# Kernel tuning notes

Hardware: AMD Instinct MI355X
Metric: run time of the kernel (lower is better)

## Reference

```python
import jax, jax.numpy as jnp
import numpy as np

N = 50_000          # nodes
E = 1_600_000       # edges (avg degree 32)
S_IN, V_IN = 128, 16
S_OUT, V_OUT = 128, 16
HID = max(V_IN, V_OUT)   # bottleneck=1 -> hidden = max(v_in, v_out)
SVO = 3                  # scalarization_vectorization_output_dim
EPS = 1e-8               # safe_norm eps


def setup_inputs() -> dict:
    key = jax.random.key(0)
    ks = jax.random.split(key, 12)
    scale = 0.05
    return {
        "scalar": jax.random.normal(ks[0], (N, S_IN), jnp.float32),
        "vector": jax.random.normal(ks[1], (N, V_IN, 3), jnp.float32),
        "edge_index": jax.random.randint(ks[2], (2, E), 0, N, jnp.int32),
        "frames": jax.random.normal(ks[3], (E, 3, 3), jnp.float32),
        # parameters (torch Linear convention: W has shape (out, in))
        "W_down": jax.random.normal(ks[4], (HID, V_IN), jnp.float32) * scale,
        "W_df": jax.random.normal(ks[5], (SVO, V_IN), jnp.float32) * scale,
        "W_so": jax.random.normal(ks[6], (S_OUT, HID + S_IN + 3 * SVO), jnp.float32) * scale,
        "b_so": jax.random.normal(ks[7], (S_OUT,), jnp.float32) * scale,
        "W_up": jax.random.normal(ks[8], (V_OUT, HID), jnp.float32) * scale,
        "W_g": jax.random.normal(ks[9], (V_OUT, S_OUT), jnp.float32) * scale,
        "b_g": jax.random.normal(ks[10], (V_OUT,), jnp.float32) * scale,
    }


def _scalarize(vdf, edge_index, frames, dim_size):
    # vdf: (N, 3xyz, SVO) node-wise down-projected vectors.
    # Gather source-node vectors per edge, rotate into each edge's local frame,
    # then scatter-mean back to source nodes (node_inputs=True path).
    row = edge_index[0]
    vi = vdf[row]                                    # (E, 3, SVO)
    local = jnp.einsum('eij,ejc->eic', frames, vi)   # project onto frame rows
    local = jnp.swapaxes(local, -1, -2).reshape(vi.shape[0], 3 * SVO)  # (E, 9)
    sums = jax.ops.segment_sum(local, row, num_segments=dim_size)
    cnt = jax.ops.segment_sum(jnp.ones((vi.shape[0],), local.dtype), row,
                              num_segments=dim_size)
    return sums / jnp.maximum(cnt, 1.0)[:, None]     # scatter mean, 0 for empty


def reference(scalar, vector, edge_index, frames,
              W_down, W_df, W_so, b_so, W_up, W_g, b_g):
    silu = jax.nn.silu
    v_pre = jnp.swapaxes(vector, -1, -2)             # (N, 3, V_IN)
    vh = v_pre @ W_down.T                            # (N, 3, HID) vector_down
    vnorm = jnp.sqrt(jnp.sum(vh * vh, axis=-2) + EPS)  # safe_norm over xyz -> (N, HID)
    vdf = v_pre @ W_df.T                             # (N, 3, SVO) vector_down_frames
    sh = _scalarize(vdf, edge_index, frames, scalar.shape[0])  # (N, 9)
    merged = jnp.concatenate([scalar, vnorm, sh], axis=-1)     # (N, S_IN+HID+9)
    s = merged @ W_so.T + b_so                       # (N, S_OUT) scalar_out
    # vector branch (vector_gate=True, frame_gate=False, no residual)
    vrep = jnp.swapaxes(vh @ W_up.T, -1, -2)         # (N, V_OUT, 3)
    gate = silu(s) @ W_g.T + b_g                     # (N, V_OUT)
    vrep = vrep * jax.nn.sigmoid(gate)[..., None]
    return silu(s), vrep
```

## Files before the change

kernel.cpp:

```cpp
#include <hip/hip_runtime.h>

typedef unsigned short ushort_t;
typedef __attribute__((ext_vector_type(4))) unsigned short bfx4;
typedef __attribute__((ext_vector_type(8))) unsigned short bfx8;
typedef __attribute__((ext_vector_type(8))) short sfx8;
typedef __attribute__((ext_vector_type(4))) float fx4;

#define NABLK  512
#define RTH    1024
#define KBMAX  52
#define CAPL   60
#define FLC    16
#define RD     6
#define QMAX   224
#define SPN    8
#define ATB    512

#define FXS 4194304.0f
#define FXONE (1 << 22)

__device__ __forceinline__ float bf2f(unsigned short u){
  unsigned int x = ((unsigned int)u) << 16;
  float f; __builtin_memcpy(&f, &x, 4); return f;
}
__device__ __forceinline__ unsigned short f2bf(float f){
  unsigned int x; __builtin_memcpy(&x, &f, 4);
  x += 0x7fffu + ((x >> 16) & 1u);
  return (unsigned short)(x >> 16);
}
__device__ __forceinline__ int f2fx(float v){ return __float2int_rn(v * FXS); }
__device__ __forceinline__ unsigned short f2h(float f){
  _Float16 h = (_Float16)f;
  unsigned short u; __builtin_memcpy(&u, &h, 2); return u;
}
__device__ __forceinline__ float h2f(unsigned int u16){
  unsigned short us = (unsigned short)u16;
  _Float16 h; __builtin_memcpy(&h, &us, 2); return (float)h;
}
__device__ __forceinline__ unsigned int pk2(float a, float b){
  return (unsigned int)f2h(a) | ((unsigned int)f2h(b) << 16);
}

__global__ __launch_bounds__(256) void k_prep(const float* __restrict__ wso,
                                              ushort_t* __restrict__ wpk,
                                              float* __restrict__ sums, int N10)
{
  int gid = blockIdx.x * 256 + threadIdx.x;
  int b4 = gid * 4;
  if (b4 + 4 <= N10){
    fx4 z = {0.f, 0.f, 0.f, 0.f};
    *(fx4*)(sums + b4) = z;
  } else if (b4 < N10){
    for (int t = b4; t < N10; t++) sums[t] = 0.f;
  }
  if (gid < 8*5*64*8){
    int j    = gid & 7;
    int lane = (gid >> 3) & 63;
    int ks   = (gid >> 9) % 5;
    int nt   = gid / 2560;
    int mrow = lane & 15, quad = lane >> 4;
    int o = nt*16 + mrow;
    int k = ks*32 + quad*8 + j;
    float v = (k < 153) ? wso[o*153 + k] : 0.f;
    wpk[gid] = f2bf(v);
  }
}

__global__ void k_edge(const int* __restrict__ ei, const float* __restrict__ frames,
                       float* __restrict__ sums, int E)
{
  int e = blockIdx.x * 256 + threadIdx.x;
  if (e >= E) return;
  int row = ei[e];
  const float* fp = frames + (size_t)e * 9;
  float F[9];
  __builtin_memcpy(F, fp, 36);
  float* sp = sums + (size_t)row * 10;
  #pragma unroll
  for (int t = 0; t < 9; t++) atomicAdd(&sp[t], F[t]);
  atomicAdd(&sp[9], 1.0f);
}

__global__ __launch_bounds__(RTH) void k_part(const int* __restrict__ ei,
                                              const float* __restrict__ frames,
                                              unsigned int* __restrict__ recs,
                                              int* __restrict__ counts,
                                              float* __restrict__ sums,
                                              int E, int EPB, int KB, int CAPG)
{
  __shared__ unsigned int s_buf[KBMAX * CAPL * RD];
  __shared__ int s_cnt[KBMAX];
  __shared__ int s_gof[KBMAX];
  __shared__ int s_cap[KBMAX];
  __shared__ int s_qb[QMAX];
  __shared__ int s_qd[QMAX];
  __shared__ int s_nq;

  const int tid  = threadIdx.x;
  const int ablk = blockIdx.x;
  const int e0 = ablk * EPB;
  const int e1 = min(e0 + EPB, E);

  for (int b = tid; b < KB; b += RTH){ s_cnt[b] = 0; s_gof[b] = 0; s_cap[b] = CAPG; }
  if (tid == 0) s_nq = 0;
  __syncthreads();

  for (int i0 = e0; i0 < e1; i0 += RTH){
    int e = i0 + tid;
    if (e < e1){
      int row = ei[e];
      float F[9];
      __builtin_memcpy(F, frames + (size_t)e * 9, 36);
      int b   = row >> 10;
      int loc = row & 1023;
      int slot = atomicAdd(&s_cnt[b], 1);
      if (slot < CAPL){
        uint2* d2 = (uint2*)(s_buf + (b * CAPL + slot) * RD);
        d2[0] = make_uint2(pk2(F[0], F[1]), pk2(F[2], F[3]));
        d2[1] = make_uint2(pk2(F[4], F[5]), pk2(F[6], F[7]));
        d2[2] = make_uint2((unsigned int)f2h(F[8]) | ((unsigned int)loc << 16), 0u);
      } else {
        float* sp = sums + (size_t)row * 10;
        #pragma unroll
        for (int t = 0; t < 9; t++) atomicAdd(&sp[t], F[t]);
        atomicAdd(&sp[9], 1.0f);
      }
    }
    __syncthreads();
    if (tid < KB){
      int c = min(s_cnt[tid], CAPL);
      int nf = c >> 4;
      int rem = c & (FLC - 1);
      if (nf > 0){
        int off = s_gof[tid];
        s_gof[tid] = off + nf * FLC;
        for (int k = 0; k < nf; k++){
          int q = atomicAdd(&s_nq, 1);
          int doff = off + k * FLC;
          s_qb[q] = (tid << 8) | (rem + k * FLC);
          if (doff + FLC <= CAPG){
            s_qd[q] = doff;
          } else {
            s_qd[q] = -1;
            s_cap[tid] = min(s_cap[tid], doff);
          }
        }
        s_cnt[tid] = rem;
      }
    }
    __syncthreads();
    const int nq = s_nq;
    for (int i = tid; i < nq * (FLC * RD); i += RTH){
      int q = i / (FLC * RD), d = i - q * (FLC * RD);
      int doff = s_qd[q];
      if (doff >= 0){
        int bb = s_qb[q] >> 8, ss = s_qb[q] & 255;
        recs[((size_t)(bb * NABLK + ablk) * CAPG + doff) * RD + d] =
            s_buf[(bb * CAPL + ss) * RD + d];
      }
    }
    for (int i = tid; i < nq * FLC; i += RTH){
      int q = i / FLC, rr = i - q * FLC;
      if (s_qd[q] < 0){
        int bb = s_qb[q] >> 8, ss = (s_qb[q] & 255) + rr;
        const unsigned int* rp = s_buf + (bb * CAPL + ss) * RD;
        int loc = rp[4] >> 16;
        float* sp = sums + (size_t)((bb << 10) + loc) * 10;
        atomicAdd(&sp[0], h2f(rp[0] & 65535u)); atomicAdd(&sp[1], h2f(rp[0] >> 16));
        atomicAdd(&sp[2], h2f(rp[1] & 65535u)); atomicAdd(&sp[3], h2f(rp[1] >> 16));
        atomicAdd(&sp[4], h2f(rp[2] & 65535u)); atomicAdd(&sp[5], h2f(rp[2] >> 16));
        atomicAdd(&sp[6], h2f(rp[3] & 65535u)); atomicAdd(&sp[7], h2f(rp[3] >> 16));
        atomicAdd(&sp[8], h2f(rp[4] & 65535u)); atomicAdd(&sp[9], 1.0f);
      }
    }
    __syncthreads();
    if (tid == 0) s_nq = 0;
  }

  for (int i = tid; i < KB * FLC; i += RTH){
    int b = i / FLC, rec = i - b * FLC;
    if (rec < s_cnt[b]){
      int off = s_gof[b] + rec;
      const unsigned int* rp = s_buf + (b * CAPL + rec) * RD;
      if (off < s_cap[b]){
        uint2* dp = (uint2*)(recs + ((size_t)(b * NABLK + ablk) * CAPG + off) * RD);
        dp[0] = make_uint2(rp[0], rp[1]);
        dp[1] = make_uint2(rp[2], rp[3]);
        dp[2] = make_uint2(rp[4], rp[5]);
      } else {
        int loc = rp[4] >> 16;
        float* sp = sums + (size_t)((b << 10) + loc) * 10;
        atomicAdd(&sp[0], h2f(rp[0] & 65535u)); atomicAdd(&sp[1], h2f(rp[0] >> 16));
        atomicAdd(&sp[2], h2f(rp[1] & 65535u)); atomicAdd(&sp[3], h2f(rp[1] >> 16));
        atomicAdd(&sp[4], h2f(rp[2] & 65535u)); atomicAdd(&sp[5], h2f(rp[2] >> 16));
        atomicAdd(&sp[6], h2f(rp[3] & 65535u)); atomicAdd(&sp[7], h2f(rp[3] >> 16));
        atomicAdd(&sp[8], h2f(rp[4] & 65535u)); atomicAdd(&sp[9], 1.0f);
      }
    }
  }
  if (tid < KB)
    counts[tid * NABLK + ablk] = min(s_gof[tid] + s_cnt[tid], s_cap[tid]);
}

__global__ __launch_bounds__(ATB) void k_accum(const unsigned int* __restrict__ recs,
                                               const int* __restrict__ counts,
                                               int* __restrict__ part, int CAPG)
{
  constexpr int APS2 = NABLK / SPN;
  __shared__ int s_pref[APS2 + 1];
  __shared__ int s_acc[1024 * 11];
  const int bucket = blockIdx.x / SPN;
  const int sp     = blockIdx.x - bucket * SPN;
  const int tid    = threadIdx.x;

  if (tid < APS2) s_pref[tid + 1] = counts[bucket * NABLK + sp * APS2 + tid];
  if (tid == 0) s_pref[0] = 0;
  for (int i = tid; i < 1024 * 11; i += ATB) s_acc[i] = 0;
  __syncthreads();
  #pragma unroll
  for (int off = 1; off < APS2; off <<= 1){
    int v = 0;
    if (tid < APS2 && tid + 1 > off) v = s_pref[tid + 1 - off];
    __syncthreads();
    if (tid < APS2) s_pref[tid + 1] += v;
    __syncthreads();
  }
  const int total = s_pref[APS2];

  for (int base = 0; base < total; base += ATB * 4){
    int got[4]; size_t ra[4];
    #pragma unroll
    for (int u = 0; u < 4; u++){
      got[u] = 0; ra[u] = 0;
      int idx = base + u * ATB + tid;
      if (idx < total){
        int lo = 0, hi = APS2;
        while (hi - lo > 1){ int mid = (lo + hi) >> 1; if (s_pref[mid] <= idx) lo = mid; else hi = mid; }
        int slot = idx - s_pref[lo];
        int ablk = sp * APS2 + lo;
        ra[u] = ((size_t)(bucket * NABLK + ablk) * CAPG + slot);
        got[u] = 1;
      }
    }
    uint2 a0[4], a1[4], a2[4];
    #pragma unroll
    for (int u = 0; u < 4; u++){
      if (got[u]){
        const unsigned int* rp = recs + ra[u] * RD;
        a0[u] = *(const uint2*)(rp + 0);
        a1[u] = *(const uint2*)(rp + 2);
        a2[u] = *(const uint2*)(rp + 4);
      }
    }
    #pragma unroll
    for (int u = 0; u < 4; u++){
      if (got[u]){
        int loc = a2[u].x >> 16;
        int* ap = s_acc + loc * 11;
        atomicAdd(&ap[0], f2fx(h2f(a0[u].x & 65535u)));
        atomicAdd(&ap[1], f2fx(h2f(a0[u].x >> 16)));
        atomicAdd(&ap[2], f2fx(h2f(a0[u].y & 65535u)));
        atomicAdd(&ap[3], f2fx(h2f(a0[u].y >> 16)));
        atomicAdd(&ap[4], f2fx(h2f(a1[u].x & 65535u)));
        atomicAdd(&ap[5], f2fx(h2f(a1[u].x >> 16)));
        atomicAdd(&ap[6], f2fx(h2f(a1[u].y & 65535u)));
        atomicAdd(&ap[7], f2fx(h2f(a1[u].y >> 16)));
        atomicAdd(&ap[8], f2fx(h2f(a2[u].x & 65535u)));
        atomicAdd(&ap[9], FXONE);
      }
    }
  }
  __syncthreads();
  int* pb = part + (size_t)(bucket * SPN + sp) * 10240;
  for (int i = tid; i < 10240; i += ATB)
    pb[i] = s_acc[(i / 10) * 11 + (i % 10)];
}

#define NPB 64
#define MS  168
#define WGS 136

__global__ __launch_bounds__(256) void k_node(
    const float* __restrict__ scalar, const float* __restrict__ vec,
    const float* __restrict__ sums,   const int* __restrict__ part,
    const float* __restrict__ wdown, const float* __restrict__ wdf,
    const ushort_t* __restrict__ wpk, const float* __restrict__ bso,
    const float* __restrict__ wup,   const float* __restrict__ wg,
    const float* __restrict__ bg,
    float* __restrict__ out0, float* __restrict__ out1, int N)
{
  __shared__ __align__(16) ushort_t sm_merged[NPB * MS];
  __shared__ __align__(16) ushort_t sm_vh[NPB * 48];
  __shared__ __align__(16) ushort_t sm_wg[16 * WGS];
  __shared__ __align__(16) ushort_t sm_wupb[512];
  __shared__ float  sm_sh[NPB * 10];
  __shared__ float  sm_vdf[NPB * 9];
  __shared__ float  sm_wd[256];
  __shared__ float  sm_wdf[48];
  __shared__ float  sm_bso[128];
  __shared__ float  sm_bg[16];

  const int tid = threadIdx.x;
  const int n0  = blockIdx.x * NPB;

  fx4 pf[8];
  #pragma unroll
  for (int it = 0; it < 8; it++){
    int idx = tid + it*256;
    int ni = idx >> 5, c4 = (idx & 31) * 4;
    int g = n0 + ni;
    fx4 z = {0.f, 0.f, 0.f, 0.f};
    pf[it] = (g < N) ? *(const fx4*)(scalar + (size_t)g*128 + c4) : z;
  }

  {
    int nv = N - n0; if (nv > NPB) nv = NPB;
    const int valid = nv * 48;
    fx4* scratch = (fx4*)sm_merged;
    for (int idx = tid; idx < NPB*48/4; idx += 256){
      fx4 val = {0.f, 0.f, 0.f, 0.f};
      if (idx*4 < valid) val = *(const fx4*)(vec + (size_t)n0*48 + idx*4);
      scratch[idx] = val;
    }
  }
  sm_wd[tid] = wdown[(tid & 15)*16 + (tid >> 4)];
  if (tid < 48) sm_wdf[tid] = wdf[tid];
  for (int idx = tid; idx < NPB*10; idx += 256){
    int ni = idx / 10, sl = idx - ni*10;
    int g = n0 + ni;
    float acc = 0.f;
    if (g < N){
      acc = sums[(size_t)g*10 + sl];
      if (part){
        int bucket = g >> 10, loc = g & 1023;
        const int* pb = part + (size_t)bucket * SPN * 10240 + loc * 10 + sl;
        int ai = 0;
        #pragma unroll
        for (int sp = 0; sp < SPN; sp++) ai += pb[(size_t)sp * 10240];
        acc += (float)ai * (1.0f / FXS);
      }
    }
    sm_sh[idx] = acc;
  }
  __syncthreads();

  #pragma unroll
  for (int it = 0; it < 4; it++){
    int idx = tid + it*256;
    int ni = idx >> 4, h = idx & 15;
    const float* sv = (const float*)sm_merged + ni*48;
    float a0 = 0.f, a1 = 0.f, a2 = 0.f;
    #pragma unroll
    for (int k = 0; k < 16; k++){
      float w = sm_wd[k*16 + h];
      a0 += sv[k*3+0]*w; a1 += sv[k*3+1]*w; a2 += sv[k*3+2]*w;
    }
    sm_vh[ni*48 +  0 + h] = f2bf(a0);
    sm_vh[ni*48 + 16 + h] = f2bf(a1);
    sm_vh[ni*48 + 32 + h] = f2bf(a2);
  }
  if (tid < NPB*3){
    const int ni = tid / 3, d = tid - ni*3;
    const float* sv = (const float*)sm_merged + ni*48;
    float c0 = 0.f, c1 = 0.f, c2 = 0.f;
    #pragma unroll
    for (int k = 0; k < 16; k++){
      float v = sv[k*3 + d];
      c0 += v * sm_wdf[ 0 + k];
      c1 += v * sm_wdf[16 + k];
      c2 += v * sm_wdf[32 + k];
    }
    sm_vdf[ni*9 + d*3 + 0] = c0;
    sm_vdf[ni*9 + d*3 + 1] = c1;
    sm_vdf[ni*9 + d*3 + 2] = c2;
  }
  __syncthreads();

  #pragma unroll
  for (int it = 0; it < 8; it++){
    int idx = tid + it*256;
    int ni = idx >> 5, c4 = (idx & 31) * 4;
    fx4 x = pf[it];
    bfx4 b; b[0]=f2bf(x[0]); b[1]=f2bf(x[1]); b[2]=f2bf(x[2]); b[3]=f2bf(x[3]);
    *(bfx4*)(sm_merged + ni*MS + c4) = b;
  }
  #pragma unroll
  for (int it = 0; it < 4; it++){
    int idx = tid + it*256;
    int ni = idx >> 4, h = idx & 15;
    float x0 = bf2f(sm_vh[ni*48 +  0 + h]);
    float x1 = bf2f(sm_vh[ni*48 + 16 + h]);
    float x2 = bf2f(sm_vh[ni*48 + 32 + h]);
    sm_merged[ni*MS + 128 + h] = f2bf(sqrtf(x0*x0 + x1*x1 + x2*x2 + 1e-8f));
  }
  for (int idx = tid; idx < NPB*9; idx += 256){
    int ni = idx / 9, t = idx - ni*9;
    int c = t / 3, i3 = (t - c*3) * 3;
    float cnt = sm_sh[ni*10 + 9];
    float inv = 1.0f / fmaxf(cnt, 1.0f);
    const float* Fs = sm_sh + ni*10;
    const float* vd = sm_vdf + ni*9;
    float val = Fs[i3+0]*vd[0*3+c] + Fs[i3+1]*vd[1*3+c] + Fs[i3+2]*vd[2*3+c];
    sm_merged[ni*MS + 144 + t] = f2bf(val * inv);
  }
  for (int idx = tid; idx < NPB*7; idx += 256){
    int ni = idx / 7, t = idx - ni*7;
    sm_merged[ni*MS + 153 + t] = 0;
  }
  for (int idx = tid; idx < 2048; idx += 256)
    sm_wg[(idx >> 7)*WGS + (idx & 127)] = f2bf(wg[idx]);
  {
    float w = wup[tid];
    unsigned short hi = f2bf(w);
    sm_wupb[tid]       = hi;
    sm_wupb[256 + tid] = f2bf(w - bf2f(hi));
  }
  if (tid < 128) sm_bso[tid] = bso[tid];
  if (tid < 16) sm_bg[tid] = bg[tid];
  __syncthreads();

  const int lane = tid & 63;
  const int wv   = tid >> 6;
  const int mrow = lane & 15;
  const int quad = lane >> 4;
  sfx8 afr[5];
  {
    const ushort_t* ab = sm_merged + (wv*16 + mrow)*MS + quad*8;
    #pragma unroll
    for (int ks = 0; ks < 5; ks++) afr[ks] = *(const sfx8*)(ab + ks*32);
  }
  const ushort_t* wb = wpk + lane*8;
  #pragma unroll
  for (int nt = 0; nt < 8; nt++){
    fx4 acc = {0.f, 0.f, 0.f, 0.f};
    #pragma unroll
    for (int ks = 0; ks < 5; ks++){
      sfx8 bfr = *(const sfx8*)(wb + (size_t)(nt*5 + ks)*64*8);
      acc = __builtin_amdgcn_mfma_f32_16x16x32_bf16(afr[ks], bfr, acc, 0, 0, 0);
    }
    const int o = nt*16 + mrow;
    const float bso_v = sm_bso[o];
    #pragma unroll
    for (int r = 0; r < 4; r++){
      int m = quad*4 + r;
      int g = n0 + wv*16 + m;
      float s = acc[r] + bso_v;
      float sact = s / (1.f + __expf(-s));
      if (g < N) out0[(size_t)g*128 + o] = sact;
      sm_merged[(wv*16 + m)*MS + o] = f2bf(sact);
    }
  }
  __syncthreads();

  {
    fx4 accg = {0.f, 0.f, 0.f, 0.f};
    const ushort_t* ga = sm_merged + (wv*16 + mrow)*MS + quad*8;
    const ushort_t* gb = sm_wg + mrow*WGS + quad*8;
    #pragma unroll
    for (int ks = 0; ks < 4; ks++){
      sfx8 af = *(const sfx8*)(ga + ks*32);
      sfx8 bf = *(const sfx8*)(gb + ks*32);
      accg = __builtin_amdgcn_mfma_f32_16x16x32_bf16(af, bf, accg, 0, 0, 0);
    }
    float sig[4];
    #pragma unroll
    for (int r = 0; r < 4; r++){
      float gv = accg[r] + sm_bg[mrow];
      sig[r] = 1.f / (1.f + __expf(-gv));
    }
    const sfx8 zero8 = {0,0,0,0,0,0,0,0};
    sfx8 bhi = zero8, blo = zero8;
    if (quad < 2){
      bhi = *(const sfx8*)(sm_wupb + mrow*16 + quad*8);
      blo = *(const sfx8*)(sm_wupb + 256 + mrow*16 + quad*8);
    }
    #pragma unroll
    for (int d = 0; d < 3; d++){
      sfx8 av = zero8;
      if (quad < 2)
        av = *(const sfx8*)(sm_vh + (wv*16 + mrow)*48 + d*16 + quad*8);
      fx4 accv = {0.f, 0.f, 0.f, 0.f};
      accv = __builtin_amdgcn_mfma_f32_16x16x32_bf16(av, blo, accv, 0, 0, 0);
      accv = __builtin_amdgcn_mfma_f32_16x16x32_bf16(av, bhi, accv, 0, 0, 0);
      #pragma unroll
      for (int r = 0; r < 4; r++){
        int m = quad*4 + r;
        int g = n0 + wv*16 + m;
        if (g < N) out1[((size_t)g*16 + mrow)*3 + d] = accv[r] * sig[r];
      }
    }
  }
}

extern "C" void kernel_launch(void* const* d_in, const int* in_sizes, int n_in,
                              void* d_out, int out_size, void* d_ws, size_t ws_size,
                              hipStream_t stream)
{
  const float* scalar = (const float*)d_in[0];
  const float* vec    = (const float*)d_in[1];
  const int*   ei     = (const int*)d_in[2];
  const float* frames = (const float*)d_in[3];
  const float* wdown  = (const float*)d_in[4];
  const float* wdf    = (const float*)d_in[5];
  const float* wso    = (const float*)d_in[6];
  const float* bso    = (const float*)d_in[7];
  const float* wup    = (const float*)d_in[8];
  const float* wg     = (const float*)d_in[9];
  const float* bg     = (const float*)d_in[10];

  const int N = in_sizes[0] / 128;
  const int E = in_sizes[2] / 2;
  const int KB  = (N + 1023) >> 10;
  const int EPB = (E + NABLK - 1) / NABLK;

  float lam = (float)EPB / (float)KB;
  int capg = (int)(lam + 3.5f * sqrtf(lam) + 17.0f);
  capg = (capg + 15) & ~15;

  char* wp = (char*)d_ws;
  float*        sums  = (float*)wp;                wp += (size_t)N * 10 * sizeof(float);
  ushort_t*     wpk   = (ushort_t*)wp;             wp += (size_t)8*5*64*8 * sizeof(ushort_t);
  int*          counts= (int*)wp;                  wp += (size_t)KB * NABLK * sizeof(int);
  unsigned int* recs  = (unsigned int*)wp;         wp += (size_t)KB * NABLK * capg * RD * sizeof(unsigned int);
  int*          part  = (int*)wp;                  wp += (size_t)KB * SPN * 10240 * sizeof(int);
  const size_t ws_needed = (size_t)(wp - (char*)d_ws);

  float* out0 = (float*)d_out;
  float* out1 = out0 + (size_t)N * 128;

  const bool binned = (ws_size >= ws_needed) && (KB <= KBMAX) && (E < (1 << 25));

  const int N10 = N * 10;
  int prepBlocks = ((N10 + 3) / 4 + 255) / 256;
  if (prepBlocks < 80) prepBlocks = 80;
  k_prep<<<prepBlocks, 256, 0, stream>>>(wso, wpk, sums, N10);

  if (binned){
    k_part<<<NABLK, RTH, 0, stream>>>(ei, frames, recs, counts, sums, E, EPB, KB, capg);
    k_accum<<<KB * SPN, ATB, 0, stream>>>(recs, counts, part, capg);
    k_node<<<(N + NPB - 1) / NPB, 256, 0, stream>>>(scalar, vec, sums, part,
                                                    wdown, wdf, wpk, bso, wup, wg, bg,
                                                    out0, out1, N);
  } else {
    k_edge<<<(E + 255) / 256, 256, 0, stream>>>(ei, frames, sums, E);
    k_node<<<(N + NPB - 1) / NPB, 256, 0, stream>>>(scalar, vec, sums, nullptr,
                                                    wdown, wdf, wpk, bso, wup, wg, bg,
                                                    out0, out1, N);
  }
}
```

Measured before the change: 207.5 us.

## Route partition overflow to per-block spill records and drop prep kernel

Edges that overflow the shared or global bucket capacity are no longer atomically added into a float sums array. They are written as packed records into a per-block overflow buffer, and k_accum then scans those buffers and folds matching records into its shared accumulators. This removes the sums array, its zeroing, and the k_prep launch in the binned path, and the weight packing moves into block 0 of k_part. The cost is an extra serial scan over all overflow lists in every k_accum block, plus the packing work on one partition block.

New measurement: 222.2 us. +7.1%, slower.

```diff
diff --git a/kernel.cpp b/kernel.cpp
--- a/kernel.cpp
+++ b/kernel.cpp
@@ -85,8 +85,11 @@
                                               const float* __restrict__ frames,
                                               unsigned int* __restrict__ recs,
                                               int* __restrict__ counts,
-                                              float* __restrict__ sums,
-                                              int E, int EPB, int KB, int CAPG)
+                                              unsigned int* __restrict__ ovrecs,
+                                              int* __restrict__ counts2,
+                                              const float* __restrict__ wso,
+                                              ushort_t* __restrict__ wpk,
+                                              int E, int EPB, int KB, int CAPG, int OVP)
 {
   __shared__ unsigned int s_buf[KBMAX * CAPL * RD];
   __shared__ int s_cnt[KBMAX];
@@ -95,14 +98,29 @@
   __shared__ int s_qb[QMAX];
   __shared__ int s_qd[QMAX];
   __shared__ int s_nq;
+  __shared__ int s_ovn;
 
   const int tid  = threadIdx.x;
   const int ablk = blockIdx.x;
   const int e0 = ablk * EPB;
   const int e1 = min(e0 + EPB, E);
 
+  if (ablk == 0){
+    for (int i = tid; i < 8*5*64*8; i += RTH){
+      int j    = i & 7;
+      int lane = (i >> 3) & 63;
+      int ks   = (i >> 9) % 5;
+      int nt   = i / 2560;
+      int mrow = lane & 15, quad = lane >> 4;
+      int o = nt*16 + mrow;
+      int k = ks*32 + quad*8 + j;
+      float v = (k < 153) ? wso[o*153 + k] : 0.f;
+      wpk[i] = f2bf(v);
+    }
+  }
+
   for (int b = tid; b < KB; b += RTH){ s_cnt[b] = 0; s_gof[b] = 0; s_cap[b] = CAPG; }
-  if (tid == 0) s_nq = 0;
+  if (tid == 0){ s_nq = 0; s_ovn = 0; }
   __syncthreads();
 
   for (int i0 = e0; i0 < e1; i0 += RTH){
@@ -120,10 +138,11 @@
         d2[1] = make_uint2(pk2(F[4], F[5]), pk2(F[6], F[7]));
         d2[2] = make_uint2((unsigned int)f2h(F[8]) | ((unsigned int)loc << 16), 0u);
       } else {
-        float* sp = sums + (size_t)row * 10;
-        #pragma unroll
-        for (int t = 0; t < 9; t++) atomicAdd(&sp[t], F[t]);
-        atomicAdd(&sp[9], 1.0f);
+        int ov = atomicAdd(&s_ovn, 1);
+        uint2* d2 = (uint2*)(ovrecs + ((size_t)ablk * OVP + ov) * RD);
+        d2[0] = make_uint2(pk2(F[0], F[1]), pk2(F[2], F[3]));
+        d2[1] = make_uint2(pk2(F[4], F[5]), pk2(F[6], F[7]));
+        d2[2] = make_uint2((unsigned int)f2h(F[8]) | ((unsigned int)row << 16), 0u);
       }
     }
     __syncthreads();
@@ -141,7 +160,8 @@
           if (doff + FLC <= CAPG){
             s_qd[q] = doff;
           } else {
-            s_qd[q] = -1;
+            int ovo = atomicAdd(&s_ovn, FLC);
+            s_qd[q] = -2 - ovo;
             s_cap[tid] = min(s_cap[tid], doff);
           }
         }
@@ -152,25 +172,19 @@
     const int nq = s_nq;
     for (int i = tid; i < nq * (FLC * RD); i += RTH){
       int q = i / (FLC * RD), d = i - q * (FLC * RD);
+      int bb = s_qb[q] >> 8, ss = s_qb[q] & 255;
       int doff = s_qd[q];
+      unsigned int v = s_buf[(bb * CAPL + ss) * RD + d];
       if (doff >= 0){
-        int bb = s_qb[q] >> 8, ss = s_qb[q] & 255;
-        recs[((size_t)(bb * NABLK + ablk) * CAPG + doff) * RD + d] =
-            s_buf[(bb * CAPL + ss) * RD + d];
-      }
-    }
-    for (int i = tid; i < nq * FLC; i += RTH){
-      int q = i / FLC, rr = i - q * FLC;
-      if (s_qd[q] < 0){
-        int bb = s_qb[q] >> 8, ss = (s_qb[q] & 255) + rr;
-        const unsigned int* rp = s_buf + (bb * CAPL + ss) * RD;
-        int loc = rp[4] >> 16;
-        float* sp = sums + (size_t)((bb << 10) + loc) * 10;
-        atomicAdd(&sp[0], h2f(rp[0] & 65535u)); atomicAdd(&sp[1], h2f(rp[0] >> 16));
-        atomicAdd(&sp[2], h2f(rp[1] & 65535u)); atomicAdd(&sp[3], h2f(rp[1] >> 16));
-        atomicAdd(&sp[4], h2f(rp[2] & 65535u)); atomicAdd(&sp[5], h2f(rp[2] >> 16));
-        atomicAdd(&sp[6], h2f(rp[3] & 65535u)); atomicAdd(&sp[7], h2f(rp[3] >> 16));
-        atomicAdd(&sp[8], h2f(rp[4] & 65535u)); atomicAdd(&sp[9], 1.0f);
+        recs[((size_t)(bb * NABLK + ablk) * CAPG + doff) * RD + d] = v;
+      } else {
+        int ovo = -2 - doff;
+        int dd = d - (d / RD) * RD;
+        if (dd == 4){
+          int loc = v >> 16;
+          v = (v & 0xFFFFu) | ((unsigned int)((bb << 10) | loc) << 16);
+        }
+        ovrecs[((size_t)ablk * OVP + ovo) * RD + d] = v;
       }
     }
     __syncthreads();
@@ -183,37 +197,44 @@
       int off = s_gof[b] + rec;
       const unsigned int* rp = s_buf + (b * CAPL + rec) * RD;
       if (off < s_cap[b]){
-        uint2* dp = (uint2*)(recs + ((size_t)(b * NABLK + ablk) * CAPG + off) * RD);
-        dp[0] = make_uint2(rp[0], rp[1]);
-        dp[1] = make_uint2(rp[2], rp[3]);
-        dp[2] = make_uint2(rp[4], rp[5]);
+        unsigned int* dp = recs + ((size_t)(b * NABLK + ablk) * CAPG + off) * RD;
+        dp[0]=rp[0]; dp[1]=rp[1]; dp[2]=rp[2]; dp[3]=rp[3]; dp[4]=rp[4]; dp[5]=rp[5];
       } else {
-        int loc = rp[4] >> 16;
-        float* sp = sums + (size_t)((b << 10) + loc) * 10;
-        atomicAdd(&sp[0], h2f(rp[0] & 65535u)); atomicAdd(&sp[1], h2f(rp[0] >> 16));
-        atomicAdd(&sp[2], h2f(rp[1] & 65535u)); atomicAdd(&sp[3], h2f(rp[1] >> 16));
-        atomicAdd(&sp[4], h2f(rp[2] & 65535u)); atomicAdd(&sp[5], h2f(rp[2] >> 16));
-        atomicAdd(&sp[6], h2f(rp[3] & 65535u)); atomicAdd(&sp[7], h2f(rp[3] >> 16));
-        atomicAdd(&sp[8], h2f(rp[4] & 65535u)); atomicAdd(&sp[9], 1.0f);
-      }
-    }
-  }
+        int ovo = atomicAdd(&s_ovn, 1);
+        unsigned int* dp = ovrecs + ((size_t)ablk * OVP + ovo) * RD;
+        dp[0]=rp[0]; dp[1]=rp[1]; dp[2]=rp[2]; dp[3]=rp[3];
+        unsigned int v4 = rp[4];
+        int loc = v4 >> 16;
+        dp[4] = (v4 & 0xFFFFu) | ((unsigned int)((b << 10) | loc) << 16);
+        dp[5] = rp[5];
+      }
+    }
+  }
+  __syncthreads();
   if (tid < KB)
     counts[tid * NABLK + ablk] = min(s_gof[tid] + s_cnt[tid], s_cap[tid]);
+  if (tid == 0)
+    counts2[ablk] = min(s_ovn, OVP);
 }
 
 __global__ __launch_bounds__(ATB) void k_accum(const unsigned int* __restrict__ recs,
                                                const int* __restrict__ counts,
-                                               int* __restrict__ part, int CAPG)
+                                               const unsigned int* __restrict__ ovrecs,
+                                               const int* __restrict__ counts2,
+                                               int* __restrict__ part, int CAPG, int OVP)
 {
   constexpr int APS2 = NABLK / SPN;
   __shared__ int s_pref[APS2 + 1];
+  __shared__ int s_c2[APS2];
   __shared__ int s_acc[1024 * 11];
   const int bucket = blockIdx.x / SPN;
   const int sp     = blockIdx.x - bucket * SPN;
   const int tid    = threadIdx.x;
 
-  if (tid < APS2) s_pref[tid + 1] = counts[bucket * NABLK + sp * APS2 + tid];
+  if (tid < APS2){
+    s_pref[tid + 1] = counts[bucket * NABLK + sp * APS2 + tid];
+    s_c2[tid]       = counts2[sp * APS2 + tid];
+  }
   if (tid == 0) s_pref[0] = 0;
   for (int i = tid; i < 1024 * 11; i += ATB) s_acc[i] = 0;
   __syncthreads();
@@ -266,6 +287,30 @@
         atomicAdd(&ap[6], f2fx(h2f(a1[u].y & 65535u)));
         atomicAdd(&ap[7], f2fx(h2f(a1[u].y >> 16)));
         atomicAdd(&ap[8], f2fx(h2f(a2[u].x & 65535u)));
+        atomicAdd(&ap[9], FXONE);
+      }
+    }
+  }
+  for (int a2i = 0; a2i < APS2; ++a2i){
+    int c2 = s_c2[a2i];
+    if (c2 == 0) continue;
+    int ablk = sp * APS2 + a2i;
+    for (int i = tid; i < c2; i += ATB){
+      const unsigned int* rp = ovrecs + ((size_t)ablk * OVP + i) * RD;
+      unsigned int r0 = rp[0], r1 = rp[1], r2 = rp[2], r3 = rp[3], r4 = rp[4];
+      int node = r4 >> 16;
+      if ((node >> 10) == bucket){
+        int loc = node & 1023;
+        int* ap = s_acc + loc * 11;
+        atomicAdd(&ap[0], f2fx(h2f(r0 & 65535u)));
+        atomicAdd(&ap[1], f2fx(h2f(r0 >> 16)));
+        atomicAdd(&ap[2], f2fx(h2f(r1 & 65535u)));
+        atomicAdd(&ap[3], f2fx(h2f(r1 >> 16)));
+        atomicAdd(&ap[4], f2fx(h2f(r2 & 65535u)));
+        atomicAdd(&ap[5], f2fx(h2f(r2 >> 16)));
+        atomicAdd(&ap[6], f2fx(h2f(r3 & 65535u)));
+        atomicAdd(&ap[7], f2fx(h2f(r3 >> 16)));
+        atomicAdd(&ap[8], f2fx(h2f(r4 & 65535u)));
         atomicAdd(&ap[9], FXONE);
       }
     }
@@ -330,7 +375,7 @@
     int g = n0 + ni;
     float acc = 0.f;
     if (g < N){
-      acc = sums[(size_t)g*10 + sl];
+      if (sums) acc = sums[(size_t)g*10 + sl];
       if (part){
         int bucket = g >> 10, loc = g & 1023;
         const int* pb = part + (size_t)bucket * SPN * 10240 + loc * 10 + sl;
@@ -516,13 +561,15 @@
   float lam = (float)EPB / (float)KB;
   int capg = (int)(lam + 3.5f * sqrtf(lam) + 17.0f);
   capg = (capg + 15) & ~15;
+  const int OVP = (EPB + FLC - 1) & ~(FLC - 1);
 
   char* wp = (char*)d_ws;
-  float*        sums  = (float*)wp;                wp += (size_t)N * 10 * sizeof(float);
-  ushort_t*     wpk   = (ushort_t*)wp;             wp += (size_t)8*5*64*8 * sizeof(ushort_t);
-  int*          counts= (int*)wp;                  wp += (size_t)KB * NABLK * sizeof(int);
-  unsigned int* recs  = (unsigned int*)wp;         wp += (size_t)KB * NABLK * capg * RD * sizeof(unsigned int);
-  int*          part  = (int*)wp;                  wp += (size_t)KB * SPN * 10240 * sizeof(int);
+  ushort_t*     wpk    = (ushort_t*)wp;            wp += (size_t)8*5*64*8 * sizeof(ushort_t);
+  int*          counts = (int*)wp;                 wp += (size_t)KB * NABLK * sizeof(int);
+  int*          counts2= (int*)wp;                 wp += (size_t)NABLK * sizeof(int);
+  unsigned int* recs   = (unsigned int*)wp;        wp += (size_t)KB * NABLK * capg * RD * sizeof(unsigned int);
+  unsigned int* ovrecs = (unsigned int*)wp;        wp += (size_t)NABLK * OVP * RD * sizeof(unsigned int);
+  int*          part   = (int*)wp;                 wp += (size_t)KB * SPN * 10240 * sizeof(int);
   const size_t ws_needed = (size_t)(wp - (char*)d_ws);
 
   float* out0 = (float*)d_out;
@@ -530,21 +577,24 @@
 
   const bool binned = (ws_size >= ws_needed) && (KB <= KBMAX) && (E < (1 << 25));
 
-  const int N10 = N * 10;
-  int prepBlocks = ((N10 + 3) / 4 + 255) / 256;
-  if (prepBlocks < 80) prepBlocks = 80;
-  k_prep<<<prepBlocks, 256, 0, stream>>>(wso, wpk, sums, N10);
-
   if (binned){
-    k_part<<<NABLK, RTH, 0, stream>>>(ei, frames, recs, counts, sums, E, EPB, KB, capg);
-    k_accum<<<KB * SPN, ATB, 0, stream>>>(recs, counts, part, capg);
-    k_node<<<(N + NPB - 1) / NPB, 256, 0, stream>>>(scalar, vec, sums, part,
+    k_part<<<NABLK, RTH, 0, stream>>>(ei, frames, recs, counts, ovrecs, counts2,
+                                      wso, wpk, E, EPB, KB, capg, OVP);
+    k_accum<<<KB * SPN, ATB, 0, stream>>>(recs, counts, ovrecs, counts2, part, capg, OVP);
+    k_node<<<(N + NPB - 1) / NPB, 256, 0, stream>>>(scalar, vec, nullptr, part,
                                                     wdown, wdf, wpk, bso, wup, wg, bg,
                                                     out0, out1, N);
   } else {
+    char* fp_ = (char*)d_ws;
+    float*    sums  = (float*)fp_;                 fp_ += (size_t)N * 10 * sizeof(float);
+    ushort_t* wpk2  = (ushort_t*)fp_;
+    const int N10 = N * 10;
+    int prepBlocks = ((N10 + 3) / 4 + 255) / 256;
+    if (prepBlocks < 80) prepBlocks = 80;
+    k_prep<<<prepBlocks, 256, 0, stream>>>(wso, wpk2, sums, N10);
     k_edge<<<(E + 255) / 256, 256, 0, stream>>>(ei, frames, sums, E);
     k_node<<<(N + NPB - 1) / NPB, 256, 0, stream>>>(scalar, vec, sums, nullptr,
-                                                    wdown, wdf, wpk, bso, wup, wg, bg,
+                                                    wdown, wdf, wpk2, bso, wup, wg, bg,
                                                     out0, out1, N);
   }
 }
```
